# Kernel tuning notes

Hardware: AMD Instinct MI355X
Metric: run time of the kernel (lower is better)

The kernel has to match this reference:

```python
import jax, jax.numpy as jnp
import numpy as np

N_NODES = 50000
N_EDGES = 600000
N_GRAPHS = 64
D_IN = 128
D_HID = 128
D_LAT = 64
BN_EPS = 1e-5


def setup_inputs() -> dict:
    key = jax.random.key(0)
    ks = jax.random.split(key, 8)
    x = jax.random.normal(ks[0], (N_NODES, D_IN), dtype=jnp.float32)
    edge_index = jax.random.randint(ks[1], (2, N_EDGES), 0, N_NODES, dtype=jnp.int64 if jax.config.jax_enable_x64 else jnp.int32)
    batch = jnp.sort(jax.random.randint(ks[2], (N_NODES,), 0, N_GRAPHS))
    d_cat = 13 * D_IN  # x + (mean,max,min,std) x (identity,amp,att)
    s = 1.0 / np.sqrt(d_cat)
    W0 = jax.random.normal(ks[3], (d_cat, D_HID), dtype=jnp.float32) * s
    W1 = jax.random.normal(ks[4], (13 * D_HID, D_HID), dtype=jnp.float32) * s
    W2 = jax.random.normal(ks[5], (13 * D_HID, D_HID), dtype=jnp.float32) * s
    fcW = jax.random.normal(ks[6], (D_HID, D_LAT), dtype=jnp.float32) * (1.0 / np.sqrt(D_HID))
    return {
        "x": x, "edge_index": edge_index, "batch": batch,
        "W0": W0, "b0": jnp.zeros((D_HID,), jnp.float32),
        "W1": W1, "b1": jnp.zeros((D_HID,), jnp.float32),
        "W2": W2, "b2": jnp.zeros((D_HID,), jnp.float32),
        "bn_gamma": jnp.ones((D_HID,), jnp.float32),
        "bn_beta": jnp.zeros((D_HID,), jnp.float32),
        "fcW": fcW, "fcb": jnp.zeros((D_LAT,), jnp.float32),
    }


def _pna_conv(h, W, b, src, dst, deg, delta):
    # h: [N, d]; messages gathered from source nodes per edge: [E, d]
    m = h[src]
    cnt = jnp.maximum(deg, 1.0)[:, None]
    ssum = jax.ops.segment_sum(m, dst, num_segments=N_NODES)
    mean = ssum / cnt
    ssq = jax.ops.segment_sum(m * m, dst, num_segments=N_NODES)
    std = jnp.sqrt(jnp.maximum(ssq / cnt - mean * mean, 0.0) + 1e-5)
    mx = jax.ops.segment_max(m, dst, num_segments=N_NODES)
    mn = jax.ops.segment_min(m, dst, num_segments=N_NODES)
    has = (deg > 0)[:, None]
    mx = jnp.where(has, mx, 0.0)
    mn = jnp.where(has, mn, 0.0)
    agg = jnp.concatenate([mean, mx, mn, std], axis=-1)  # [N, 4d]
    logd = jnp.log(deg + 1.0)[:, None]
    amp = logd / delta
    att = delta / jnp.maximum(logd, 1e-5)
    feat = jnp.concatenate([h, agg, agg * amp, agg * att], axis=-1)  # [N, 13d]
    return feat @ W + b


def reference(x, edge_index, batch, W0, b0, W1, b1, W2, b2, bn_gamma, bn_beta, fcW, fcb):
    src, dst = edge_index[0], edge_index[1]
    deg = jax.ops.segment_sum(jnp.ones((src.shape[0],), x.dtype), dst, num_segments=N_NODES)
    delta = jnp.mean(jnp.log(deg + 1.0))  # avg log-degree normalizer
    h = jax.nn.relu(_pna_conv(x, W0, b0, src, dst, deg, delta))
    h = jax.nn.relu(_pna_conv(h, W1, b1, src, dst, deg, delta))
    h = jax.nn.relu(_pna_conv(h, W2, b2, src, dst, deg, delta))
    # dropout is identity in eval mode
    pooled = jax.ops.segment_sum(h, batch, num_segments=N_GRAPHS)  # global_add_pool
    mu = jnp.mean(pooled, axis=0)
    var = jnp.var(pooled, axis=0)
    bn = (pooled - mu) / jnp.sqrt(var + BN_EPS) * bn_gamma + bn_beta
    return bn @ fcW + fcb
```

## Files before the change

### kernel.cpp

```cpp
#include <hip/hip_runtime.h>
#include <cstdint>
#include <cstddef>

#define N_NODESC 50000
#define N_PAD    50048
#define N_EDGESC 600000
#define N_GRAPHSC 64
#define D_HIDC   128
#define D_LATC   64
#define D_GS     512
#define D_WROW   1664

typedef unsigned short u16;
typedef unsigned int   u32;

typedef _Float16 f16x8 __attribute__((ext_vector_type(8)));
typedef _Float16 f16x2 __attribute__((ext_vector_type(2)));
typedef float    f32x4 __attribute__((ext_vector_type(4)));
typedef float    f32x2 __attribute__((ext_vector_type(2)));

__device__ __forceinline__ u16 f2h(float f) {
    return __builtin_bit_cast(u16, (_Float16)f);
}
__device__ __forceinline__ float h2f(u16 u) {
    return (float)__builtin_bit_cast(_Float16, u);
}
__device__ __forceinline__ u32 pkrtz(float a, float b) {
    return __builtin_bit_cast(u32, __builtin_amdgcn_cvt_pkrtz(a, b));
}

__device__ __forceinline__ f32x2 pk_add(f32x2 a, f32x2 b) {
    f32x2 d;
    asm("v_pk_add_f32 %0, %1, %2" : "=v"(d) : "v"(a), "v"(b));
    return d;
}
__device__ __forceinline__ f32x2 pk_fma(f32x2 a, f32x2 b, f32x2 c) {
    f32x2 d;
    asm("v_pk_fma_f32 %0, %1, %2, %3" : "=v"(d) : "v"(a), "v"(b), "v"(c));
    return d;
}

__device__ __forceinline__ void gll16(void* lds, const void* g) {
    __builtin_amdgcn_global_load_lds(
        (const __attribute__((address_space(1))) void*)g,
        (__attribute__((address_space(3))) void*)lds, 16, 0, 0);
}

__global__ void __launch_bounds__(256) k_setup(
        const float* __restrict__ x, const float* __restrict__ W0,
        const float* __restrict__ W1, const float* __restrict__ W2,
        const int* __restrict__ batch,
        u16* __restrict__ h, u16* __restrict__ Wt,
        int* __restrict__ zero_base, int nz, int ZB, int* __restrict__ goff) {
    __shared__ u16 lt[64 * 128];
    int b = blockIdx.x;
    int t = threadIdx.x;
    if (b < ZB) {
        int i = b * 256 + t;
        if (i < nz) zero_base[i] = 0;
        return;
    }
    b -= ZB;
    if (b < 12500) {
        int i = b * 256 + t;
        float2 v = ((const float2*)x)[i];
        ((u32*)h)[i] = (u32)f2h(v.x) | ((u32)f2h(v.y) << 16);
        return;
    }
    b -= 12500;
    if (b < 78) {
        int which = b / 26;
        int k0 = (b % 26) * 64;
        const float* W = (which == 0) ? W0 : (which == 1) ? W1 : W2;
        const float* src = W + (size_t)k0 * D_HIDC;
        for (int i = t; i < 64 * 128; i += 256)
            lt[i] = f2h(src[i]);
        __syncthreads();
        int j = t & 127, kh = t >> 7;
        u16* dst = Wt + (size_t)which * D_WROW * D_HIDC
                      + (size_t)j * D_WROW + k0 + kh * 32;
        #pragma unroll
        for (int c = 0; c < 4; c++) {
            int kb = kh * 32 + c * 8;
            u32 p0 = (u32)lt[(kb + 0) * 128 + j] | ((u32)lt[(kb + 1) * 128 + j] << 16);
            u32 p1 = (u32)lt[(kb + 2) * 128 + j] | ((u32)lt[(kb + 3) * 128 + j] << 16);
            u32 p2 = (u32)lt[(kb + 4) * 128 + j] | ((u32)lt[(kb + 5) * 128 + j] << 16);
            u32 p3 = (u32)lt[(kb + 6) * 128 + j] | ((u32)lt[(kb + 7) * 128 + j] << 16);
            uint4 v; v.x = p0; v.y = p1; v.z = p2; v.w = p3;
            *(uint4*)(dst + c * 8) = v;
        }
        return;
    }
    int g = t;
    if (g <= N_GRAPHSC) {
        int lo = 0, hi = N_NODESC;
        while (lo < hi) {
            int mid = (lo + hi) >> 1;
            if (batch[mid] < g) lo = mid + 1; else hi = mid;
        }
        goff[g] = lo;
    }
}

__global__ void k_count(const int* __restrict__ dst, int* __restrict__ deg) {
    int e = blockIdx.x * 256 + threadIdx.x;
    if (e < N_EDGESC) atomicAdd(&deg[dst[e]], 1);
}

__global__ void __launch_bounds__(256) k_scan_part(
        const int* __restrict__ deg, int* __restrict__ bsum,
        float* __restrict__ lsum) {
    __shared__ int s[256];
    __shared__ float ls[256];
    int idx = blockIdx.x * 256 + threadIdx.x;
    int v = (idx < N_NODESC) ? deg[idx] : 0;
    s[threadIdx.x] = v;
    ls[threadIdx.x] = (idx < N_NODESC) ? logf((float)v + 1.0f) : 0.0f;
    __syncthreads();
    for (int o = 128; o > 0; o >>= 1) {
        if (threadIdx.x < o) {
            s[threadIdx.x] += s[threadIdx.x + o];
            ls[threadIdx.x] += ls[threadIdx.x + o];
        }
        __syncthreads();
    }
    if (threadIdx.x == 0) { bsum[blockIdx.x] = s[0]; lsum[blockIdx.x] = ls[0]; }
}

__global__ void __launch_bounds__(256) k_scan_block(
        int* __restrict__ bsum, const float* __restrict__ lsum,
        float* __restrict__ delta_p) {
    __shared__ int s[256];
    __shared__ float ls[256];
    int t = threadIdx.x;
    int v = (t < 196) ? bsum[t] : 0;
    s[t] = v;
    ls[t] = (t < 196) ? lsum[t] : 0.0f;
    __syncthreads();
    for (int o = 1; o < 256; o <<= 1) {
        int add = (t >= o) ? s[t - o] : 0;
        __syncthreads();
        s[t] += add;
        __syncthreads();
    }
    if (t < 196) bsum[t] = s[t] - v;
    for (int o = 128; o > 0; o >>= 1) {
        if (t < o) ls[t] += ls[t + o];
        __syncthreads();
    }
    if (t == 0) delta_p[0] = ls[0] * (1.0f / (float)N_NODESC);
}

__global__ void __launch_bounds__(256) k_scan_final(
        const int* __restrict__ deg, const int* __restrict__ bsum,
        int* __restrict__ row_off) {
    __shared__ int s[256];
    int t = threadIdx.x;
    int idx = blockIdx.x * 256 + t;
    int v = (idx < N_NODESC) ? deg[idx] : 0;
    s[t] = v; __syncthreads();
    for (int o = 1; o < 256; o <<= 1) {
        int add = (t >= o) ? s[t - o] : 0;
        __syncthreads();
        s[t] += add;
        __syncthreads();
    }
    int excl = s[t] - v + bsum[blockIdx.x];
    if (idx < N_NODESC) row_off[idx] = excl;
    if (idx == 0) row_off[N_NODESC] = N_EDGESC;
}

__global__ void k_fill_csr(const int* __restrict__ src, const int* __restrict__ dst,
                           const int* __restrict__ row_off, int* __restrict__ cursor,
                           int* __restrict__ csr_src) {
    int e = blockIdx.x * 256 + threadIdx.x;
    if (e < N_EDGESC) {
        int d = dst[e];
        int pos = row_off[d] + atomicAdd(&cursor[d], 1);
        csr_src[pos] = src[e] << 8;
    }
}


__global__ void __launch_bounds__(256) k_aggregate(
        const u16* __restrict__ h, const int* __restrict__ row_off,
        const int* __restrict__ csr_src, u16* __restrict__ G) {
    int lane = threadIdx.x & 63;
    int half = lane >> 5, l32 = lane & 31;
    int n = blockIdx.x * 8 + ((threadIdx.x >> 6) << 1) + half;
    if (n >= N_NODESC) return;
    int c4 = 4 * l32;
    u32 c8 = 8u * (u32)l32;
    const char* h8 = (const char*)h;
    int beg = row_off[n], end = row_off[n + 1];
    const _Float16 NEG = (_Float16)(-65504.0f), POS = (_Float16)(65504.0f);
    f32x2 s01 = {0.f, 0.f}, s23 = {0.f, 0.f};
    f32x2 q01 = {0.f, 0.f}, q23 = {0.f, 0.f};
    f16x2 mx01 = {NEG, NEG}, mx23 = {NEG, NEG};
    f16x2 mn01 = {POS, POS}, mn23 = {POS, POS};

    #define PROC(u) { \
        f16x2 p01 = __builtin_bit_cast(f16x2, (u).x); \
        f16x2 p23 = __builtin_bit_cast(f16x2, (u).y); \
        f32x2 c01 = __builtin_convertvector(p01, f32x2); \
        f32x2 c23 = __builtin_convertvector(p23, f32x2); \
        s01 = pk_add(s01, c01); s23 = pk_add(s23, c23); \
        q01 = pk_fma(c01, c01, q01); q23 = pk_fma(c23, c23, q23); \
        mx01 = __builtin_elementwise_max(mx01, p01); \
        mx23 = __builtin_elementwise_max(mx23, p23); \
        mn01 = __builtin_elementwise_min(mn01, p01); \
        mn23 = __builtin_elementwise_min(mn23, p23); }
    #define GTH(e) (*(const uint2*)(h8 + ((e) + c8)))

    int i = beg;
    if (i + 8 <= end) {
        u32 e0 = (u32)csr_src[i],     e1 = (u32)csr_src[i + 1];
        u32 e2 = (u32)csr_src[i + 2], e3 = (u32)csr_src[i + 3];
        u32 e4 = (u32)csr_src[i + 4], e5 = (u32)csr_src[i + 5];
        u32 e6 = (u32)csr_src[i + 6], e7 = (u32)csr_src[i + 7];
        while (i + 16 <= end) {
            uint2 u0 = GTH(e0), u1 = GTH(e1), u2 = GTH(e2), u3 = GTH(e3);
            uint2 u4 = GTH(e4), u5 = GTH(e5), u6 = GTH(e6), u7 = GTH(e7);
            e0 = (u32)csr_src[i + 8];  e1 = (u32)csr_src[i + 9];
            e2 = (u32)csr_src[i + 10]; e3 = (u32)csr_src[i + 11];
            e4 = (u32)csr_src[i + 12]; e5 = (u32)csr_src[i + 13];
            e6 = (u32)csr_src[i + 14]; e7 = (u32)csr_src[i + 15];
            PROC(u0); PROC(u1); PROC(u2); PROC(u3);
            PROC(u4); PROC(u5); PROC(u6); PROC(u7);
            i += 8;
        }
        uint2 u0 = GTH(e0), u1 = GTH(e1), u2 = GTH(e2), u3 = GTH(e3);
        uint2 u4 = GTH(e4), u5 = GTH(e5), u6 = GTH(e6), u7 = GTH(e7);
        PROC(u0); PROC(u1); PROC(u2); PROC(u3);
        PROC(u4); PROC(u5); PROC(u6); PROC(u7);
        i += 8;
    }
    for (; i + 3 < end; i += 4) {
        u32 e0 = (u32)csr_src[i],     e1 = (u32)csr_src[i + 1];
        u32 e2 = (u32)csr_src[i + 2], e3 = (u32)csr_src[i + 3];
        uint2 u0 = GTH(e0), u1 = GTH(e1), u2 = GTH(e2), u3 = GTH(e3);
        PROC(u0); PROC(u1); PROC(u2); PROC(u3);
    }
    for (; i < end; ++i) {
        u32 e0 = (u32)csr_src[i];
        uint2 u0 = GTH(e0);
        PROC(u0);
    }
    #undef PROC
    #undef GTH

    int d = end - beg;
    float inv = 1.0f / fmaxf((float)d, 1.0f);
    f32x2 vinv = {inv, inv};
    f32x2 me01 = s01 * vinv, me23 = s23 * vinv;
    f32x2 qn01 = q01 * vinv, qn23 = q23 * vinv;
    f32x2 var01 = qn01 - me01 * me01;
    f32x2 var23 = qn23 - me23 * me23;
    const f32x2 z2 = {0.f, 0.f};
    var01 = __builtin_elementwise_max(var01, z2);
    var23 = __builtin_elementwise_max(var23, z2);
    float sd0 = sqrtf(var01.x + 1e-5f), sd1 = sqrtf(var01.y + 1e-5f);
    float sd2 = sqrtf(var23.x + 1e-5f), sd3 = sqrtf(var23.y + 1e-5f);

    u32 mep01 = pkrtz(me01.x, me01.y), mep23 = pkrtz(me23.x, me23.y);
    u32 sdp01 = pkrtz(sd0, sd1),       sdp23 = pkrtz(sd2, sd3);
    u32 mxb01 = __builtin_bit_cast(u32, mx01), mxb23 = __builtin_bit_cast(u32, mx23);
    u32 mnb01 = __builtin_bit_cast(u32, mn01), mnb23 = __builtin_bit_cast(u32, mn23);
    if (d == 0) { mxb01 = mxb23 = mnb01 = mnb23 = 0u; }

    u16* base = G + (size_t)n * D_GS;
    uint2 M; M.x = mep01; M.y = mep23;
    uint2 X; X.x = mxb01; X.y = mxb23;
    uint2 N_; N_.x = mnb01; N_.y = mnb23;
    uint2 S; S.x = sdp01; S.y = sdp23;
    *(uint2*)(base + c4)       = M;
    *(uint2*)(base + 128 + c4) = X;
    *(uint2*)(base + 256 + c4) = N_;
    *(uint2*)(base + 384 + c4) = S;
}

__global__ void __launch_bounds__(256, 2) k_gemm(
        const u16* __restrict__ hin, const u16* __restrict__ G,
        const u16* __restrict__ Wt,
        const int* __restrict__ deg, const float* __restrict__ delta_p,
        const float* __restrict__ bias, u16* __restrict__ hout) {
    __shared__ _Float16 A1[128 * 64];
    __shared__ _Float16 A2[128 * 64];
    __shared__ _Float16 A3[128 * 64];
    __shared__ _Float16 Bt[128 * 64];
    const _Float16* Wf = (const _Float16*)Wt;
    const _Float16* Gf = (const _Float16*)G;
    const _Float16* Hf = (const _Float16*)hin;
    int n0 = blockIdx.x * 128;
    int t = threadIdx.x;
    int w = t >> 6, lane = t & 63;
    int srow8 = lane >> 3, sslot = lane & 7;
    int stg = (sslot ^ srow8) * 8;
    int q4 = lane >> 4, r16 = lane & 15;
    int sx0 = (q4 ^ (lane & 7)) * 8;
    int sx1 = ((q4 + 4) ^ (lane & 7)) * 8;
    int col = lane & 15;

    float delta = delta_p[0];
    float atv[8];
    _Float16 amh[8];
    #pragma unroll
    for (int nt = 0; nt < 8; nt++) {
        int node = n0 + nt * 16 + col;
        float logd = logf((float)deg[node] + 1.0f);
        amh[nt] = (_Float16)(logd / delta);
        atv[nt] = delta / fmaxf(logd, 1e-5f);
    }

    f32x4 acc[2][8], ac3[2][8];
    #pragma unroll
    for (int a = 0; a < 2; a++)
        #pragma unroll
        for (int b = 0; b < 8; b++) {
            acc[a][b] = (f32x4){0.f, 0.f, 0.f, 0.f};
            ac3[a][b] = (f32x4){0.f, 0.f, 0.f, 0.f};
        }

    for (int ki = 0; ki < 10; ki++) {
        int k0 = ki * 64;
        bool sreg = (k0 >= 128);
        __syncthreads();
        #pragma unroll
        for (int r = 0; r < 4; r++) {
            int rr = r * 4 + w;
            const _Float16* wrow = Wf + (size_t)(rr * 8 + srow8) * D_WROW;
            gll16(&A1[rr * 512], wrow + k0 + stg);
        }
        if (sreg) {
            #pragma unroll
            for (int r = 0; r < 4; r++) {
                int rr = r * 4 + w;
                const _Float16* wrow = Wf + (size_t)(rr * 8 + srow8) * D_WROW;
                gll16(&A2[rr * 512], wrow + 512 + k0 + stg);
                gll16(&A3[rr * 512], wrow + 1024 + k0 + stg);
            }
        }
        #pragma unroll
        for (int q = 0; q < 4; q++) {
            int rr = q * 4 + w;
            int row = n0 + rr * 8 + srow8;
            const _Float16* bsrc = (!sreg)
                ? Hf + (size_t)row * D_HIDC + k0 + stg
                : Gf + (size_t)row * D_GS + (k0 - 128) + stg;
            gll16(&Bt[rr * 512], bsrc);
        }
        __syncthreads();
        f16x8 a00 = *(const f16x8*)&A1[(w * 32 + r16) * 64 + sx0];
        f16x8 a01 = *(const f16x8*)&A1[(w * 32 + r16) * 64 + sx1];
        f16x8 a10 = *(const f16x8*)&A1[(w * 32 + 16 + r16) * 64 + sx0];
        f16x8 a11 = *(const f16x8*)&A1[(w * 32 + 16 + r16) * 64 + sx1];
        if (!sreg) {
            #pragma unroll
            for (int nt = 0; nt < 8; nt++) {
                f16x8 b0 = *(const f16x8*)&Bt[(nt * 16 + r16) * 64 + sx0];
                f16x8 b1 = *(const f16x8*)&Bt[(nt * 16 + r16) * 64 + sx1];
                acc[0][nt] = __builtin_amdgcn_mfma_f32_16x16x32_f16(a00, b0, acc[0][nt], 0, 0, 0);
                acc[1][nt] = __builtin_amdgcn_mfma_f32_16x16x32_f16(a10, b0, acc[1][nt], 0, 0, 0);
                acc[0][nt] = __builtin_amdgcn_mfma_f32_16x16x32_f16(a01, b1, acc[0][nt], 0, 0, 0);
                acc[1][nt] = __builtin_amdgcn_mfma_f32_16x16x32_f16(a11, b1, acc[1][nt], 0, 0, 0);
            }
        } else {
            f16x8 w2a0 = *(const f16x8*)&A2[(w * 32 + r16) * 64 + sx0];
            f16x8 w2a1 = *(const f16x8*)&A2[(w * 32 + r16) * 64 + sx1];
            f16x8 w2b0 = *(const f16x8*)&A2[(w * 32 + 16 + r16) * 64 + sx0];
            f16x8 w2b1 = *(const f16x8*)&A2[(w * 32 + 16 + r16) * 64 + sx1];
            f16x8 w3a0 = *(const f16x8*)&A3[(w * 32 + r16) * 64 + sx0];
            f16x8 w3a1 = *(const f16x8*)&A3[(w * 32 + r16) * 64 + sx1];
            f16x8 w3b0 = *(const f16x8*)&A3[(w * 32 + 16 + r16) * 64 + sx0];
            f16x8 w3b1 = *(const f16x8*)&A3[(w * 32 + 16 + r16) * 64 + sx1];
            #pragma unroll
            for (int nt = 0; nt < 8; nt++) {
                f16x8 b0 = *(const f16x8*)&Bt[(nt * 16 + r16) * 64 + sx0];
                f16x8 b1 = *(const f16x8*)&Bt[(nt * 16 + r16) * 64 + sx1];
                f16x8 bm0 = b0 * amh[nt];
                f16x8 bm1 = b1 * amh[nt];
                acc[0][nt] = __builtin_amdgcn_mfma_f32_16x16x32_f16(a00, b0, acc[0][nt], 0, 0, 0);
                acc[1][nt] = __builtin_amdgcn_mfma_f32_16x16x32_f16(a10, b0, acc[1][nt], 0, 0, 0);
                acc[0][nt] = __builtin_amdgcn_mfma_f32_16x16x32_f16(a01, b1, acc[0][nt], 0, 0, 0);
                acc[1][nt] = __builtin_amdgcn_mfma_f32_16x16x32_f16(a11, b1, acc[1][nt], 0, 0, 0);
                acc[0][nt] = __builtin_amdgcn_mfma_f32_16x16x32_f16(w2a0, bm0, acc[0][nt], 0, 0, 0);
                acc[1][nt] = __builtin_amdgcn_mfma_f32_16x16x32_f16(w2b0, bm0, acc[1][nt], 0, 0, 0);
                acc[0][nt] = __builtin_amdgcn_mfma_f32_16x16x32_f16(w2a1, bm1, acc[0][nt], 0, 0, 0);
                acc[1][nt] = __builtin_amdgcn_mfma_f32_16x16x32_f16(w2b1, bm1, acc[1][nt], 0, 0, 0);
                ac3[0][nt] = __builtin_amdgcn_mfma_f32_16x16x32_f16(w3a0, b0, ac3[0][nt], 0, 0, 0);
                ac3[1][nt] = __builtin_amdgcn_mfma_f32_16x16x32_f16(w3b0, b0, ac3[1][nt], 0, 0, 0);
                ac3[0][nt] = __builtin_amdgcn_mfma_f32_16x16x32_f16(w3a1, b1, ac3[0][nt], 0, 0, 0);
                ac3[1][nt] = __builtin_amdgcn_mfma_f32_16x16x32_f16(w3b1, b1, ac3[1][nt], 0, 0, 0);
            }
        }
    }
    int rowq = q4 * 4;
    #pragma unroll
    for (int nt = 0; nt < 8; nt++) {
        int node = n0 + nt * 16 + col;
        float at = atv[nt];
        #pragma unroll
        for (int mt = 0; mt < 2; mt++) {
            int jb = w * 32 + mt * 16 + rowq;
            f32x4 v = acc[mt][nt], v3 = ac3[mt][nt];
            ushort4 o;
            o.x = f2h(fmaxf(v.x + at * v3.x + bias[jb], 0.0f));
            o.y = f2h(fmaxf(v.y + at * v3.y + bias[jb + 1], 0.0f));
            o.z = f2h(fmaxf(v.z + at * v3.z + bias[jb + 2], 0.0f));
            o.w = f2h(fmaxf(v.w + at * v3.w + bias[jb + 3], 0.0f));
            *(ushort4*)&hout[(size_t)node * D_HIDC + jb] = o;
        }
    }
}


__global__ void __launch_bounds__(256) k_pool(
        const u16* __restrict__ h, const int* __restrict__ goff,
        float* __restrict__ pooled) {
    __shared__ float sm[256];
    int g = blockIdx.x >> 2, s = blockIdx.x & 3;
    int gb = goff[g], ge = goff[g + 1];
    int len = ge - gb;
    int q = (len + 3) >> 2;
    int nb = gb + s * q;
    int ne = min(nb + q, ge);
    int t = threadIdx.x;
    int j = t & 127, half = t >> 7;
    float acc = 0.0f;
    for (int n = nb + half; n < ne; n += 2)
        acc += h2f(h[(size_t)n * D_HIDC + j]);
    sm[t] = acc; __syncthreads();
    if (t < 128) {
        float v = sm[t] + sm[t + 128];
        atomicAdd(&pooled[g * D_HIDC + j], v);
    }
}

__global__ void __launch_bounds__(128) k_bn_fc(
        const float* __restrict__ pooled, const float* __restrict__ gamma,
        const float* __restrict__ beta, const float* __restrict__ fcW,
        const float* __restrict__ fcb, float* __restrict__ out) {
    __shared__ float bn[D_HIDC];
    int g = blockIdx.x, t = threadIdx.x;
    float s = 0.f, q = 0.f;
    for (int gg = 0; gg < N_GRAPHSC; gg++) {
        float v = pooled[gg * D_HIDC + t];
        s += v; q += v * v;
    }
    float mu = s * (1.0f / N_GRAPHSC);
    float var = q * (1.0f / N_GRAPHSC) - mu * mu;
    float inv = 1.0f / sqrtf(var + 1e-5f);
    bn[t] = (pooled[g * D_HIDC + t] - mu) * inv * gamma[t] + beta[t];
    __syncthreads();
    if (t < D_LATC) {
        float accum = fcb[t];
        for (int j = 0; j < D_HIDC; j++) accum += bn[j] * fcW[j * D_LATC + t];
        out[g * D_LATC + t] = accum;
    }
}


extern "C" void kernel_launch(void* const* d_in, const int* in_sizes, int n_in,
                              void* d_out, int out_size, void* d_ws, size_t ws_size,
                              hipStream_t stream) {
    const float* x     = (const float*)d_in[0];
    const int*   ei    = (const int*)d_in[1];
    const int*   batch = (const int*)d_in[2];
    const float* W0 = (const float*)d_in[3];
    const float* b0 = (const float*)d_in[4];
    const float* W1 = (const float*)d_in[5];
    const float* b1 = (const float*)d_in[6];
    const float* W2 = (const float*)d_in[7];
    const float* b2 = (const float*)d_in[8];
    const float* gamma = (const float*)d_in[9];
    const float* beta  = (const float*)d_in[10];
    const float* fcW   = (const float*)d_in[11];
    const float* fcb   = (const float*)d_in[12];
    float* out = (float*)d_out;
    const int* srcv = ei;
    const int* dstv = ei + N_EDGESC;

    char* p = (char*)d_ws;
    auto alloc = [&](size_t bytes) -> char* {
        char* r = p;
        p += (bytes + 255) & ~(size_t)255;
        return r;
    };
    int*   deg_cnt = (int*)alloc((size_t)N_PAD * 4);
    int*   cursor  = (int*)alloc((size_t)N_NODESC * 4);
    float* delta_p = (float*)alloc(4);
    float* pooled  = (float*)alloc((size_t)N_GRAPHSC * D_HIDC * 4);
    char*  zero_end = p;
    int*   row_off = (int*)alloc((size_t)(N_NODESC + 1) * 4);
    int*   goff    = (int*)alloc((size_t)(N_GRAPHSC + 1) * 4);
    int*   bsum    = (int*)alloc(256 * 4);
    float* lsum    = (float*)alloc(256 * 4);
    int*   csr_src = (int*)alloc((size_t)N_EDGESC * 4);
    u16*   Wt      = (u16*)alloc((size_t)3 * D_WROW * D_HIDC * 2);
    u16*   hA      = (u16*)alloc((size_t)N_PAD * D_HIDC * 2);
    u16*   hB      = (u16*)alloc((size_t)N_PAD * D_HIDC * 2);
    u16*   G       = (u16*)alloc((size_t)N_PAD * D_GS * 2);

    int nz = (int)((zero_end - (char*)deg_cnt) / 4);
    int ZB = (nz + 255) / 256;
    int setup_grid = ZB + 12500 + 78 + 1;
    k_setup<<<setup_grid, 256, 0, stream>>>(x, W0, W1, W2, batch,
                                            hB, Wt, deg_cnt, nz, ZB, goff);
    k_count<<<(N_EDGESC + 255) / 256, 256, 0, stream>>>(dstv, deg_cnt);
    k_scan_part<<<196, 256, 0, stream>>>(deg_cnt, bsum, lsum);
    k_scan_block<<<1, 256, 0, stream>>>(bsum, lsum, delta_p);
    k_scan_final<<<196, 256, 0, stream>>>(deg_cnt, bsum, row_off);
    k_fill_csr<<<(N_EDGESC + 255) / 256, 256, 0, stream>>>(srcv, dstv, row_off, cursor, csr_src);

    const float* bs[3] = {b0, b1, b2};
    const u16* h_in[3]  = {hB, hA, hB};
    u16*       h_out[3] = {hA, hB, hA};
    size_t wsz = (size_t)D_WROW * D_HIDC;
    for (int l = 0; l < 3; l++) {
        k_aggregate<<<(N_NODESC + 7) / 8, 256, 0, stream>>>(
            h_in[l], row_off, csr_src, G);
        k_gemm<<<N_PAD / 128, 256, 0, stream>>>(
            h_in[l], G, Wt + (size_t)l * wsz, deg_cnt, delta_p, bs[l], h_out[l]);
    }
    k_pool<<<4 * N_GRAPHSC, 256, 0, stream>>>(h_out[2], goff, pooled);
    k_bn_fc<<<N_GRAPHSC, 128, 0, stream>>>(pooled, gamma, beta, fcW, fcb, out);
}
```

Measured before the change: 378.5 us.

## Fuse neighbor aggregation into per-layer GEMM kernel

Merges the separate aggregation kernel into the GEMM kernel, so each block first aggregates its 128 nodes (each half-wave handles 16 nodes in sequence) and writes G, then syncs and runs the GEMM on those rows. This removes one launch per layer and lets the GEMM read G rows that were just written and are likely still in cache. In exchange, aggregation parallelism drops from about 6250 small blocks to 391 blocks at occupancy 2, with a serial per-node loop that can expose gather latency and load imbalance.

```diff
diff --git a/kernel.cpp b/kernel.cpp
--- a/kernel.cpp
+++ b/kernel.cpp
@@ -182,117 +182,120 @@
 }
 
 
-__global__ void __launch_bounds__(256) k_aggregate(
-        const u16* __restrict__ h, const int* __restrict__ row_off,
-        const int* __restrict__ csr_src, u16* __restrict__ G) {
-    int lane = threadIdx.x & 63;
-    int half = lane >> 5, l32 = lane & 31;
-    int n = blockIdx.x * 8 + ((threadIdx.x >> 6) << 1) + half;
-    if (n >= N_NODESC) return;
-    int c4 = 4 * l32;
-    u32 c8 = 8u * (u32)l32;
-    const char* h8 = (const char*)h;
-    int beg = row_off[n], end = row_off[n + 1];
-    const _Float16 NEG = (_Float16)(-65504.0f), POS = (_Float16)(65504.0f);
-    f32x2 s01 = {0.f, 0.f}, s23 = {0.f, 0.f};
-    f32x2 q01 = {0.f, 0.f}, q23 = {0.f, 0.f};
-    f16x2 mx01 = {NEG, NEG}, mx23 = {NEG, NEG};
-    f16x2 mn01 = {POS, POS}, mn23 = {POS, POS};
-
-    #define PROC(u) { \
-        f16x2 p01 = __builtin_bit_cast(f16x2, (u).x); \
-        f16x2 p23 = __builtin_bit_cast(f16x2, (u).y); \
-        f32x2 c01 = __builtin_convertvector(p01, f32x2); \
-        f32x2 c23 = __builtin_convertvector(p23, f32x2); \
-        s01 = pk_add(s01, c01); s23 = pk_add(s23, c23); \
-        q01 = pk_fma(c01, c01, q01); q23 = pk_fma(c23, c23, q23); \
-        mx01 = __builtin_elementwise_max(mx01, p01); \
-        mx23 = __builtin_elementwise_max(mx23, p23); \
-        mn01 = __builtin_elementwise_min(mn01, p01); \
-        mn23 = __builtin_elementwise_min(mn23, p23); }
-    #define GTH(e) (*(const uint2*)(h8 + ((e) + c8)))
-
-    int i = beg;
-    if (i + 8 <= end) {
-        u32 e0 = (u32)csr_src[i],     e1 = (u32)csr_src[i + 1];
-        u32 e2 = (u32)csr_src[i + 2], e3 = (u32)csr_src[i + 3];
-        u32 e4 = (u32)csr_src[i + 4], e5 = (u32)csr_src[i + 5];
-        u32 e6 = (u32)csr_src[i + 6], e7 = (u32)csr_src[i + 7];
-        while (i + 16 <= end) {
-            uint2 u0 = GTH(e0), u1 = GTH(e1), u2 = GTH(e2), u3 = GTH(e3);
-            uint2 u4 = GTH(e4), u5 = GTH(e5), u6 = GTH(e6), u7 = GTH(e7);
-            e0 = (u32)csr_src[i + 8];  e1 = (u32)csr_src[i + 9];
-            e2 = (u32)csr_src[i + 10]; e3 = (u32)csr_src[i + 11];
-            e4 = (u32)csr_src[i + 12]; e5 = (u32)csr_src[i + 13];
-            e6 = (u32)csr_src[i + 14]; e7 = (u32)csr_src[i + 15];
-            PROC(u0); PROC(u1); PROC(u2); PROC(u3);
-            PROC(u4); PROC(u5); PROC(u6); PROC(u7);
-            i += 8;
-        }
-        uint2 u0 = GTH(e0), u1 = GTH(e1), u2 = GTH(e2), u3 = GTH(e3);
-        uint2 u4 = GTH(e4), u5 = GTH(e5), u6 = GTH(e6), u7 = GTH(e7);
-        PROC(u0); PROC(u1); PROC(u2); PROC(u3);
-        PROC(u4); PROC(u5); PROC(u6); PROC(u7);
-        i += 8;
-    }
-    for (; i + 3 < end; i += 4) {
-        u32 e0 = (u32)csr_src[i],     e1 = (u32)csr_src[i + 1];
-        u32 e2 = (u32)csr_src[i + 2], e3 = (u32)csr_src[i + 3];
-        uint2 u0 = GTH(e0), u1 = GTH(e1), u2 = GTH(e2), u3 = GTH(e3);
-        PROC(u0); PROC(u1); PROC(u2); PROC(u3);
-    }
-    for (; i < end; ++i) {
-        u32 e0 = (u32)csr_src[i];
-        uint2 u0 = GTH(e0);
-        PROC(u0);
-    }
-    #undef PROC
-    #undef GTH
-
-    int d = end - beg;
-    float inv = 1.0f / fmaxf((float)d, 1.0f);
-    f32x2 vinv = {inv, inv};
-    f32x2 me01 = s01 * vinv, me23 = s23 * vinv;
-    f32x2 qn01 = q01 * vinv, qn23 = q23 * vinv;
-    f32x2 var01 = qn01 - me01 * me01;
-    f32x2 var23 = qn23 - me23 * me23;
-    const f32x2 z2 = {0.f, 0.f};
-    var01 = __builtin_elementwise_max(var01, z2);
-    var23 = __builtin_elementwise_max(var23, z2);
-    float sd0 = sqrtf(var01.x + 1e-5f), sd1 = sqrtf(var01.y + 1e-5f);
-    float sd2 = sqrtf(var23.x + 1e-5f), sd3 = sqrtf(var23.y + 1e-5f);
-
-    u32 mep01 = pkrtz(me01.x, me01.y), mep23 = pkrtz(me23.x, me23.y);
-    u32 sdp01 = pkrtz(sd0, sd1),       sdp23 = pkrtz(sd2, sd3);
-    u32 mxb01 = __builtin_bit_cast(u32, mx01), mxb23 = __builtin_bit_cast(u32, mx23);
-    u32 mnb01 = __builtin_bit_cast(u32, mn01), mnb23 = __builtin_bit_cast(u32, mn23);
-    if (d == 0) { mxb01 = mxb23 = mnb01 = mnb23 = 0u; }
-
-    u16* base = G + (size_t)n * D_GS;
-    uint2 M; M.x = mep01; M.y = mep23;
-    uint2 X; X.x = mxb01; X.y = mxb23;
-    uint2 N_; N_.x = mnb01; N_.y = mnb23;
-    uint2 S; S.x = sdp01; S.y = sdp23;
-    *(uint2*)(base + c4)       = M;
-    *(uint2*)(base + 128 + c4) = X;
-    *(uint2*)(base + 256 + c4) = N_;
-    *(uint2*)(base + 384 + c4) = S;
-}
-
-__global__ void __launch_bounds__(256, 2) k_gemm(
-        const u16* __restrict__ hin, const u16* __restrict__ G,
+__global__ void __launch_bounds__(256, 2) k_layer(
+        const u16* __restrict__ hin, u16* __restrict__ G,
         const u16* __restrict__ Wt,
         const int* __restrict__ deg, const float* __restrict__ delta_p,
-        const float* __restrict__ bias, u16* __restrict__ hout) {
+        const float* __restrict__ bias,
+        const int* __restrict__ row_off, const int* __restrict__ csr_src,
+        u16* __restrict__ hout) {
     __shared__ _Float16 A1[128 * 64];
     __shared__ _Float16 A2[128 * 64];
     __shared__ _Float16 A3[128 * 64];
     __shared__ _Float16 Bt[128 * 64];
+    int n0 = blockIdx.x * 128;
+    int t = threadIdx.x;
+
+    {
+        int hw = t >> 5, l32 = t & 31;
+        int c4 = 4 * l32;
+        u32 c8 = 8u * (u32)l32;
+        const char* h8 = (const char*)hin;
+        const _Float16 NEG = (_Float16)(-65504.0f), POS = (_Float16)(65504.0f);
+        for (int s16 = 0; s16 < 16; s16++) {
+            int n = n0 + hw * 16 + s16;
+            if (n >= N_NODESC) continue;
+            int beg = row_off[n], end = row_off[n + 1];
+            f32x2 s01 = {0.f, 0.f}, s23 = {0.f, 0.f};
+            f32x2 q01 = {0.f, 0.f}, q23 = {0.f, 0.f};
+            f16x2 mx01 = {NEG, NEG}, mx23 = {NEG, NEG};
+            f16x2 mn01 = {POS, POS}, mn23 = {POS, POS};
+
+            #define PROC(u) { \
+                f16x2 p01 = __builtin_bit_cast(f16x2, (u).x); \
+                f16x2 p23 = __builtin_bit_cast(f16x2, (u).y); \
+                f32x2 c01 = __builtin_convertvector(p01, f32x2); \
+                f32x2 c23 = __builtin_convertvector(p23, f32x2); \
+                s01 = pk_add(s01, c01); s23 = pk_add(s23, c23); \
+                q01 = pk_fma(c01, c01, q01); q23 = pk_fma(c23, c23, q23); \
+                mx01 = __builtin_elementwise_max(mx01, p01); \
+                mx23 = __builtin_elementwise_max(mx23, p23); \
+                mn01 = __builtin_elementwise_min(mn01, p01); \
+                mn23 = __builtin_elementwise_min(mn23, p23); }
+            #define GTH(e) (*(const uint2*)(h8 + ((e) + c8)))
+
+            int i = beg;
+            if (i + 8 <= end) {
+                u32 e0 = (u32)csr_src[i],     e1 = (u32)csr_src[i + 1];
+                u32 e2 = (u32)csr_src[i + 2], e3 = (u32)csr_src[i + 3];
+                u32 e4 = (u32)csr_src[i + 4], e5 = (u32)csr_src[i + 5];
+                u32 e6 = (u32)csr_src[i + 6], e7 = (u32)csr_src[i + 7];
+                while (i + 16 <= end) {
+                    uint2 u0 = GTH(e0), u1 = GTH(e1), u2 = GTH(e2), u3 = GTH(e3);
+                    uint2 u4 = GTH(e4), u5 = GTH(e5), u6 = GTH(e6), u7 = GTH(e7);
+                    e0 = (u32)csr_src[i + 8];  e1 = (u32)csr_src[i + 9];
+                    e2 = (u32)csr_src[i + 10]; e3 = (u32)csr_src[i + 11];
+                    e4 = (u32)csr_src[i + 12]; e5 = (u32)csr_src[i + 13];
+                    e6 = (u32)csr_src[i + 14]; e7 = (u32)csr_src[i + 15];
+                    PROC(u0); PROC(u1); PROC(u2); PROC(u3);
+                    PROC(u4); PROC(u5); PROC(u6); PROC(u7);
+                    i += 8;
+                }
+                uint2 u0 = GTH(e0), u1 = GTH(e1), u2 = GTH(e2), u3 = GTH(e3);
+                uint2 u4 = GTH(e4), u5 = GTH(e5), u6 = GTH(e6), u7 = GTH(e7);
+                PROC(u0); PROC(u1); PROC(u2); PROC(u3);
+                PROC(u4); PROC(u5); PROC(u6); PROC(u7);
+                i += 8;
+            }
+            for (; i + 3 < end; i += 4) {
+                u32 e0 = (u32)csr_src[i],     e1 = (u32)csr_src[i + 1];
+                u32 e2 = (u32)csr_src[i + 2], e3 = (u32)csr_src[i + 3];
+                uint2 u0 = GTH(e0), u1 = GTH(e1), u2 = GTH(e2), u3 = GTH(e3);
+                PROC(u0); PROC(u1); PROC(u2); PROC(u3);
+            }
+            for (; i < end; ++i) {
+                u32 e0 = (u32)csr_src[i];
+                uint2 u0 = GTH(e0);
+                PROC(u0);
+            }
+            #undef PROC
+            #undef GTH
+
+            int d = end - beg;
+            float inv = 1.0f / fmaxf((float)d, 1.0f);
+            f32x2 vinv = {inv, inv};
+            f32x2 me01 = s01 * vinv, me23 = s23 * vinv;
+            f32x2 qn01 = q01 * vinv, qn23 = q23 * vinv;
+            f32x2 var01 = qn01 - me01 * me01;
+            f32x2 var23 = qn23 - me23 * me23;
+            const f32x2 z2 = {0.f, 0.f};
+            var01 = __builtin_elementwise_max(var01, z2);
+            var23 = __builtin_elementwise_max(var23, z2);
+            float sd0 = sqrtf(var01.x + 1e-5f), sd1 = sqrtf(var01.y + 1e-5f);
+            float sd2 = sqrtf(var23.x + 1e-5f), sd3 = sqrtf(var23.y + 1e-5f);
+
+            u32 mep01 = pkrtz(me01.x, me01.y), mep23 = pkrtz(me23.x, me23.y);
+            u32 sdp01 = pkrtz(sd0, sd1),       sdp23 = pkrtz(sd2, sd3);
+            u32 mxb01 = __builtin_bit_cast(u32, mx01), mxb23 = __builtin_bit_cast(u32, mx23);
+            u32 mnb01 = __builtin_bit_cast(u32, mn01), mnb23 = __builtin_bit_cast(u32, mn23);
+            if (d == 0) { mxb01 = mxb23 = mnb01 = mnb23 = 0u; }
+
+            u16* base = G + (size_t)n * D_GS;
+            uint2 M; M.x = mep01; M.y = mep23;
+            uint2 X; X.x = mxb01; X.y = mxb23;
+            uint2 N_; N_.x = mnb01; N_.y = mnb23;
+            uint2 S; S.x = sdp01; S.y = sdp23;
+            *(uint2*)(base + c4)       = M;
+            *(uint2*)(base + 128 + c4) = X;
+            *(uint2*)(base + 256 + c4) = N_;
+            *(uint2*)(base + 384 + c4) = S;
+        }
+    }
+    __syncthreads();
+
     const _Float16* Wf = (const _Float16*)Wt;
     const _Float16* Gf = (const _Float16*)G;
     const _Float16* Hf = (const _Float16*)hin;
-    int n0 = blockIdx.x * 128;
-    int t = threadIdx.x;
     int w = t >> 6, lane = t & 63;
     int srow8 = lane >> 3, sslot = lane & 7;
     int stg = (sslot ^ srow8) * 8;
@@ -517,10 +520,9 @@
     u16*       h_out[3] = {hA, hB, hA};
     size_t wsz = (size_t)D_WROW * D_HIDC;
     for (int l = 0; l < 3; l++) {
-        k_aggregate<<<(N_NODESC + 7) / 8, 256, 0, stream>>>(
-            h_in[l], row_off, csr_src, G);
-        k_gemm<<<N_PAD / 128, 256, 0, stream>>>(
-            h_in[l], G, Wt + (size_t)l * wsz, deg_cnt, delta_p, bs[l], h_out[l]);
+        k_layer<<<N_PAD / 128, 256, 0, stream>>>(
+            h_in[l], G, Wt + (size_t)l * wsz, deg_cnt, delta_p, bs[l],
+            row_off, csr_src, h_out[l]);
     }
     k_pool<<<4 * N_GRAPHSC, 256, 0, stream>>>(h_out[2], goff, pooled);
     k_bn_fc<<<N_GRAPHSC, 128, 0, stream>>>(pooled, gamma, beta, fcW, fcb, out);
```

Result: slower. 477.2 us (+26.1%).
